# Performance work log

Measured on AMD Instinct MI355X. Metric: run time of the kernel, lower is better.

## Reference

```python
import jax, jax.numpy as jnp
import numpy as np


def setup_inputs() -> dict:
    key = jax.random.key(0)
    k0, k1, k2, k3 = jax.random.split(key, 4)
    B, in_dim, n_vars, out_dim, E = 64, 512, 512, 720, 8
    x = jax.random.normal(k0, (B, in_dim, n_vars), dtype=jnp.float32)
    # Gating: nn.Linear(in_dim, E, bias=False) -> weight [E, in_dim]
    Wg = jax.random.normal(k1, (E, in_dim), dtype=jnp.float32) * 0.02
    # Experts: nn.Linear(in_dim, out_dim) -> weight [out_dim, in_dim], bias [out_dim]
    We = jax.random.normal(k2, (E, out_dim, in_dim), dtype=jnp.float32) * 0.02
    be = jax.random.normal(k3, (E, out_dim), dtype=jnp.float32) * 0.02
    return {"x": x, "Wg": Wg, "We": We, "be": be, "top_k": 2}


def reference(x, Wg, We, be, top_k):
    # x: [B, in_len, n_vars] -> tokens along n_vars with feature dim in_len
    xt = jnp.swapaxes(x, 1, 2)                      # [B, V, D]
    gate = jax.nn.softmax(xt @ Wg.T, axis=-1)       # [B, V, E]
    weights, sel = jax.lax.top_k(gate, top_k)       # [B, V, k]
    E, O, D = We.shape
    out = jnp.zeros(xt.shape[:2] + (O,), dtype=xt.dtype)  # [B, V, O]
    for e in range(E):
        # combine weight for expert e: sum over top-k slots routed to e
        coef = jnp.sum(jnp.where(sel == e, weights, jnp.zeros_like(weights)), axis=-1)  # [B, V]
        out = out + coef[..., None] * (jnp.einsum('bvd,od->bvo', xt, We[e]) + be[e])
    return jnp.swapaxes(out, 1, 2)                  # [B, pred_len, n_vars]
```

## Files before the change

### kernel.cpp

```cpp
#include <hip/hip_runtime.h>
#include <hip/hip_bf16.h>

#define DID 512
#define NV  512
#define NB  64
#define OD  720
#define OPAD 768
#define NE  8
#define NTOK (NB * NV)
#define MAXTILE 512

typedef short  bf16x8 __attribute__((ext_vector_type(8)));
typedef float  f32x4  __attribute__((ext_vector_type(4)));

#define XT_OFF    0u
#define WB_OFF    33554432u
#define PID_OFF   39845888u
#define C1D_OFF   39976960u
#define C2D_OFF   40108032u
#define TL_OFF    40239104u
#define CL1_OFF   40370176u
#define CL2_OFF   40501248u
#define BCNT_OFF  40632320u
#define BFILL_OFF 40632576u
#define BOFF_OFF  40632832u
#define TPID_OFF  40633088u
#define TT0_OFF   40635136u
#define TEND_OFF  40637184u
#define NT_OFF    40639232u
#define SCR_OFF   40639488u
#define SCR_END   87825408u

static __device__ __forceinline__ ushort f2bf(float f) {
  unsigned u = __float_as_uint(f);
  unsigned r = (u + 0x7fffu + ((u >> 16) & 1u)) >> 16;
  return (ushort)r;
}
static __device__ __forceinline__ float bf2f(ushort u) {
  return __uint_as_float(((unsigned)u) << 16);
}
static __device__ __forceinline__ void async16(const ushort* g, ushort* l) {
  __builtin_amdgcn_global_load_lds((__attribute__((address_space(1))) void*)(g),
                                   (__attribute__((address_space(3))) void*)(l),
                                   16, 0, 0);
}

__global__ __launch_bounds__(256) void k_prep(const float* __restrict__ x,
                                              ushort* __restrict__ xt,
                                              const float* __restrict__ We,
                                              ushort* __restrict__ wb,
                                              int* __restrict__ bcnt) {
  const int tid = threadIdx.x;
  if (blockIdx.z < 64) {
    if (blockIdx.z == 0 && blockIdx.x == 0 && blockIdx.y == 0 && tid < 128)
      bcnt[tid] = 0;
    __shared__ float s[32][33];
    const int b  = blockIdx.z;
    const int v0 = blockIdx.x * 32;
    const int d0 = blockIdx.y * 32;
    const int tx = tid & 31;
    const int ty = tid >> 5;
    const float* xp = x + ((size_t)b * DID + d0 + ty) * NV + v0 + tx;
#pragma unroll
    for (int i = 0; i < 4; ++i) s[ty + i * 8][tx] = xp[(size_t)i * 8 * NV];
    __syncthreads();
#pragma unroll
    for (int i = 0; i < 4; ++i) {
      int vl = ty + i * 8;
      xt[((size_t)b * NV + v0 + vl) * DID + d0 + tx] = f2bf(s[tx][vl]);
    }
  } else {
    const int e = blockIdx.z - 64;
    int i = (blockIdx.y * 16 + blockIdx.x) * 256 + tid;
    for (; i < OPAD * DID; i += 65536) {
      const int o = i >> 9;
      ushort val = 0;
      if (o < OD) val = f2bf(We[(size_t)e * OD * DID + i]);
      wb[(size_t)e * OPAD * DID + i] = val;
    }
  }
}

__global__ __launch_bounds__(256) void k_gate(const float* __restrict__ x,
                                              const float* __restrict__ Wg,
                                              int* __restrict__ pairid,
                                              float* __restrict__ c1d,
                                              float* __restrict__ c2d,
                                              int* __restrict__ bcnt) {
  __shared__ float wg[NE * DID];
  __shared__ int cnt64[64];
  const int tid = threadIdx.x;
  for (int i = tid; i < NE * DID; i += 256) wg[i] = Wg[i];
  if (tid < 64) cnt64[tid] = 0;
  __syncthreads();

  const int b = blockIdx.y;
  const int v = blockIdx.x * 256 + tid;
  const float* xp = x + (size_t)b * DID * NV + v;

  float acc[NE];
#pragma unroll
  for (int e = 0; e < NE; ++e) acc[e] = 0.f;
  for (int d = 0; d < DID; d += 4) {
    float x0 = xp[(size_t)(d + 0) * NV];
    float x1 = xp[(size_t)(d + 1) * NV];
    float x2 = xp[(size_t)(d + 2) * NV];
    float x3 = xp[(size_t)(d + 3) * NV];
#pragma unroll
    for (int e = 0; e < NE; ++e) {
      float4 w4 = *(const float4*)&wg[e * DID + d];
      acc[e] += x0 * w4.x + x1 * w4.y + x2 * w4.z + x3 * w4.w;
    }
  }
  float mx = acc[0];
#pragma unroll
  for (int e = 1; e < NE; ++e) mx = fmaxf(mx, acc[e]);
  float sum = 0.f;
#pragma unroll
  for (int e = 0; e < NE; ++e) { acc[e] = __expf(acc[e] - mx); sum += acc[e]; }
  const float inv = 1.f / sum;

  int i1 = 0; float g1 = acc[0];
#pragma unroll
  for (int e = 1; e < NE; ++e) if (acc[e] > g1) { g1 = acc[e]; i1 = e; }
  int i2 = -1; float g2 = -1.f;
#pragma unroll
  for (int e = 0; e < NE; ++e) if (e != i1 && acc[e] > g2) { g2 = acc[e]; i2 = e; }
  g1 *= inv; g2 *= inv;

  int ea, eb; float ca, cb;
  if (i1 < i2) { ea = i1; eb = i2; ca = g1; cb = g2; }
  else         { ea = i2; eb = i1; ca = g2; cb = g1; }
  const int pid = ea * 8 + eb;
  const int t = b * NV + v;
  pairid[t] = pid; c1d[t] = ca; c2d[t] = cb;
  atomicAdd(&cnt64[pid], 1);
  __syncthreads();
  if (tid < 64 && cnt64[tid]) atomicAdd(&bcnt[tid], cnt64[tid]);
}

__global__ void k_prefix(const int* __restrict__ bcnt, int* __restrict__ boffs,
                         int* __restrict__ tpid, int* __restrict__ tt0,
                         int* __restrict__ tend, int* __restrict__ ntp) {
  const int p = threadIdx.x;
  const int c = bcnt[p];
  int inc = c;
#pragma unroll
  for (int d = 1; d < 64; d <<= 1) {
    int n = __shfl_up(inc, d, 64);
    if (p >= d) inc += n;
  }
  const int off = inc - c;
  boffs[p] = off;
  const int tc = (c + 127) >> 7;
  int inct = tc;
#pragma unroll
  for (int d = 1; d < 64; d <<= 1) {
    int n = __shfl_up(inct, d, 64);
    if (p >= d) inct += n;
  }
  const int tb = inct - tc;
  for (int i = 0; i < tc; ++i) {
    tpid[tb + i] = p; tt0[tb + i] = off + i * 128; tend[tb + i] = off + c;
  }
  if (p == 63) ntp[0] = inct;
}

__global__ __launch_bounds__(256) void k_scatter(const int* __restrict__ pairid,
                                                 const float* __restrict__ c1d,
                                                 const float* __restrict__ c2d,
                                                 const int* __restrict__ boffs,
                                                 int* __restrict__ bfill,
                                                 int* __restrict__ tlist,
                                                 float* __restrict__ cl1,
                                                 float* __restrict__ cl2) {
  __shared__ int cnt64[64], base64[64];
  const int tid = threadIdx.x;
  if (tid < 64) cnt64[tid] = 0;
  __syncthreads();
  const int t = blockIdx.x * 256 + tid;
  const int pid = pairid[t];
  const int p = atomicAdd(&cnt64[pid], 1);
  __syncthreads();
  if (tid < 64) base64[tid] = cnt64[tid] ? atomicAdd(&bfill[tid], cnt64[tid]) : 0;
  __syncthreads();
  const int slot = boffs[pid] + base64[pid] + p;
  tlist[slot] = t; cl1[slot] = c1d[t]; cl2[slot] = c2d[t];
}

__global__ __launch_bounds__(256, 2) void k_gemm(
    const ushort* __restrict__ xt, const ushort* __restrict__ wb,
    const float* __restrict__ be, const int* __restrict__ tlist,
    const float* __restrict__ cl1, const float* __restrict__ cl2,
    const int* __restrict__ tpid, const int* __restrict__ tt0,
    const int* __restrict__ tendarr, const int* __restrict__ ntp,
    ushort* __restrict__ scratch, float* __restrict__ out, int mode) {
  const int tile = blockIdx.y;
  if (tile >= ntp[0]) return;
  const int pid  = tpid[tile];
  const int t0   = tt0[tile];
  const int tend = tendarr[tile];
  const int e1 = pid >> 3, e2 = pid & 7;
  const int o0 = blockIdx.x * 128;

  __shared__ __align__(16) ushort As[2][4096];
  __shared__ __align__(16) ushort Bs[2][4096];

  const int tid  = threadIdx.x;
  const int lane = tid & 63;
  const int w    = tid >> 6;
  const int m16  = lane & 15;
  const int ch   = lane >> 4;

  const int rA0 = 2 * w * 16 + m16;
  const int sl0 = t0 + rA0, sl1 = sl0 + 16;
  const int tk0 = (sl0 < tend) ? tlist[sl0] : 0;
  const int tk1 = (sl1 < tend) ? tlist[sl1] : 0;

  const size_t eStride = (size_t)OPAD * DID;
  const int    aoff    = (o0 + rA0) * DID + ch * 8;
  const ushort* gb0 = xt + (size_t)tk0 * DID + ch * 8;
  const ushort* gb1 = xt + (size_t)tk1 * DID + ch * 8;

  const int dst0 = 2 * w * 512 + lane * 8;
  const int dst1 = dst0 + 512;

  const int m    = lane & 15;
  const int quad = lane >> 4;
  const int wo   = (w >> 1) * 64;
  const int wt   = (w & 1) * 64;
  const int fa   = (w >> 1) * 4;
  const int fb   = (w & 1) * 4;

  f32x4 acc[4][4];
#pragma unroll
  for (int i = 0; i < 4; ++i)
#pragma unroll
    for (int j = 0; j < 4; ++j) acc[i][j] = (f32x4){0.f, 0.f, 0.f, 0.f};

  {
    const ushort* wA = wb + (size_t)e1 * eStride + aoff;
    async16(wA, &As[0][dst0]);
    async16(wA + 16 * DID, &As[0][dst1]);
    async16(gb0, &Bs[0][dst0]);
    async16(gb1, &Bs[0][dst1]);
  }

  for (int kk = 0; kk < 32; ++kk) {
    __syncthreads();

    if (kk == 16) {
      float ratio[4];
#pragma unroll
      for (int j = 0; j < 4; ++j) {
        const int sl = t0 + wt + j * 16 + m;
        const bool g = sl < tend;
        const float cc1 = g ? cl1[sl] : 0.f;
        const float cc2 = g ? cl2[sl] : 1.f;
        ratio[j] = cc1 / cc2;
      }
      const float* be1p = be + e1 * OD;
#pragma unroll
      for (int i = 0; i < 4; ++i) {
        const int ob = o0 + wo + i * 16 + quad * 4;
        float b0 = 0, b1 = 0, b2 = 0, b3 = 0;
        if (ob < OD) { b0 = be1p[ob]; b1 = be1p[ob + 1]; b2 = be1p[ob + 2]; b3 = be1p[ob + 3]; }
#pragma unroll
        for (int j = 0; j < 4; ++j) {
          acc[i][j][0] = (acc[i][j][0] + b0) * ratio[j];
          acc[i][j][1] = (acc[i][j][1] + b1) * ratio[j];
          acc[i][j][2] = (acc[i][j][2] + b2) * ratio[j];
          acc[i][j][3] = (acc[i][j][3] + b3) * ratio[j];
        }
      }
    }

    const int nk = kk + 1;
    if (nk < 32) {
      const int nb = nk & 1;
      const int eA = (nk < 16) ? e1 : e2;
      const int k0 = (nk & 15) * 32;
      const ushort* wA = wb + (size_t)eA * eStride + aoff + k0;
      async16(wA, &As[nb][dst0]);
      async16(wA + 16 * DID, &As[nb][dst1]);
      async16(gb0 + k0, &Bs[nb][dst0]);
      async16(gb1 + k0, &Bs[nb][dst1]);
    }

    const int cb = kk & 1;
    bf16x8 af[4], bfr[4];
#pragma unroll
    for (int i = 0; i < 4; ++i)
      af[i] = *(const bf16x8*)(&As[cb][(fa + i) * 512 + lane * 8]);
#pragma unroll
    for (int j = 0; j < 4; ++j)
      bfr[j] = *(const bf16x8*)(&Bs[cb][(fb + j) * 512 + lane * 8]);
#pragma unroll
    for (int i = 0; i < 4; ++i)
#pragma unroll
      for (int j = 0; j < 4; ++j)
        acc[i][j] = __builtin_amdgcn_mfma_f32_16x16x32_bf16(af[i], bfr[j],
                                                            acc[i][j], 0, 0, 0);
  }

  float c2v[4]; int tokv[4]; bool gv[4];
#pragma unroll
  for (int j = 0; j < 4; ++j) {
    const int sl = t0 + wt + j * 16 + m;
    gv[j] = sl < tend;
    c2v[j]  = gv[j] ? cl2[sl] : 0.f;
    tokv[j] = gv[j] ? tlist[sl] : 0;
  }
  const float* be2p = be + e2 * OD;
#pragma unroll
  for (int i = 0; i < 4; ++i) {
    const int ob = o0 + wo + i * 16 + quad * 4;
    if (ob < OD) {
      const float b0 = be2p[ob], b1 = be2p[ob + 1], b2 = be2p[ob + 2], b3 = be2p[ob + 3];
#pragma unroll
      for (int j = 0; j < 4; ++j) {
        if (gv[j]) {
          const float v0 = c2v[j] * (acc[i][j][0] + b0);
          const float v1 = c2v[j] * (acc[i][j][1] + b1);
          const float v2 = c2v[j] * (acc[i][j][2] + b2);
          const float v3 = c2v[j] * (acc[i][j][3] + b3);
          if (mode == 0) {
            ushort4 pk = make_ushort4(f2bf(v0), f2bf(v1), f2bf(v2), f2bf(v3));
            *(ushort4*)(scratch + (size_t)tokv[j] * OD + ob) = pk;
          } else {
            const int bb = tokv[j] >> 9, vv = tokv[j] & 511;
            float* op = out + ((size_t)bb * OD + ob) * NV + vv;
            op[0] = v0; op[(size_t)NV] = v1; op[2 * (size_t)NV] = v2; op[3 * (size_t)NV] = v3;
          }
        }
      }
    }
  }
}

__global__ __launch_bounds__(256) void k_combine(const ushort* __restrict__ scratch,
                                                 float* __restrict__ out) {
  __shared__ ushort s[64][68];
  const int v0 = blockIdx.x * 64;
  const int o0 = blockIdx.y * 64;
  const int b  = blockIdx.z;
  const int tid = threadIdx.x;
#pragma unroll
  for (int it = 0; it < 2; ++it) {
    const int c = it * 256 + tid;
    const int row = c >> 3, cg = c & 7;
    const int o = o0 + cg * 8;
    if (o + 8 <= OD) {
      const ushort* src = scratch + ((size_t)(b * NV + v0 + row)) * OD + o;
      ushort4 ua = *(const ushort4*)(src);
      ushort4 ub = *(const ushort4*)(src + 4);
      *(ushort4*)&s[row][cg * 8] = ua;
      *(ushort4*)&s[row][cg * 8 + 4] = ub;
    }
  }
  __syncthreads();
  const int vv = tid & 63;
  const int og = tid >> 6;
#pragma unroll
  for (int oi = 0; oi < 8; ++oi) {
    const int ol = (og * 8 + oi) * 2;
    const int o = o0 + ol;
    if (o < OD) {
      ushort2 u = *(const ushort2*)&s[vv][ol];
      float* op = out + ((size_t)b * OD + o) * NV + v0 + vv;
      op[0]  = bf2f(u.x);
      op[NV] = bf2f(u.y);
    }
  }
}

extern "C" void kernel_launch(void* const* d_in, const int* in_sizes, int n_in,
                              void* d_out, int out_size, void* d_ws, size_t ws_size,
                              hipStream_t stream) {
  const float* x  = (const float*)d_in[0];
  const float* Wg = (const float*)d_in[1];
  const float* We = (const float*)d_in[2];
  const float* be = (const float*)d_in[3];
  float* out = (float*)d_out;

  char* ws = (char*)d_ws;
  ushort* xt     = (ushort*)(ws + XT_OFF);
  ushort* wb     = (ushort*)(ws + WB_OFF);
  int*    pairid = (int*)   (ws + PID_OFF);
  float*  c1d    = (float*) (ws + C1D_OFF);
  float*  c2d    = (float*) (ws + C2D_OFF);
  int*    tlist  = (int*)   (ws + TL_OFF);
  float*  cl1    = (float*) (ws + CL1_OFF);
  float*  cl2    = (float*) (ws + CL2_OFF);
  int*    bcnt   = (int*)   (ws + BCNT_OFF);
  int*    bfill  = (int*)   (ws + BFILL_OFF);
  int*    boffs  = (int*)   (ws + BOFF_OFF);
  int*    tpid   = (int*)   (ws + TPID_OFF);
  int*    tt0    = (int*)   (ws + TT0_OFF);
  int*    tend   = (int*)   (ws + TEND_OFF);
  int*    ntp    = (int*)   (ws + NT_OFF);
  ushort* scratch= (ushort*)(ws + SCR_OFF);

  const int mode = (ws_size >= (size_t)SCR_END) ? 0 : 1;

  k_prep<<<dim3(16, 16, 72), 256, 0, stream>>>(x, xt, We, wb, bcnt);
  k_gate<<<dim3(NV / 256, NB), 256, 0, stream>>>(x, Wg, pairid, c1d, c2d, bcnt);
  k_prefix<<<1, 64, 0, stream>>>(bcnt, boffs, tpid, tt0, tend, ntp);
  k_scatter<<<NTOK / 256, 256, 0, stream>>>(pairid, c1d, c2d, boffs, bfill,
                                            tlist, cl1, cl2);
  k_gemm<<<dim3(OPAD / 128, 320), 256, 0, stream>>>(xt, wb, be, tlist, cl1, cl2,
                                                    tpid, tt0, tend, ntp,
                                                    scratch, out, mode);
  if (mode == 0)
    k_combine<<<dim3(NV / 64, (OD + 63) / 64, NB), 256, 0, stream>>>(scratch, out);
}
```

Before: 359.2 us.

## Write GEMM output directly, drop bf16 scratch combine pass, widen transpose tiles

Drops the bf16 scratch buffer and the separate combine/transpose kernel. The GEMM epilogue now always scatters fp32 results straight into the transposed output. The grid is swapped so that consecutive blocks walk token tiles instead of output columns. The x transpose-and-convert in k_prep moves to 64x64 tiles with 4-wide packed bf16 stores, and the We conversion uses fewer blocks. This trades the extra kernel launch and the scratch round trip for strided, uncoalesced fp32 stores from the GEMM.

```diff
diff --git a/kernel.cpp b/kernel.cpp
--- a/kernel.cpp
+++ b/kernel.cpp
@@ -28,16 +28,11 @@
 #define TT0_OFF   40635136u
 #define TEND_OFF  40637184u
 #define NT_OFF    40639232u
-#define SCR_OFF   40639488u
-#define SCR_END   87825408u
 
 static __device__ __forceinline__ ushort f2bf(float f) {
   unsigned u = __float_as_uint(f);
   unsigned r = (u + 0x7fffu + ((u >> 16) & 1u)) >> 16;
   return (ushort)r;
-}
-static __device__ __forceinline__ float bf2f(ushort u) {
-  return __uint_as_float(((unsigned)u) << 16);
 }
 static __device__ __forceinline__ void async16(const ushort* g, ushort* l) {
   __builtin_amdgcn_global_load_lds((__attribute__((address_space(1))) void*)(g),
@@ -54,25 +49,30 @@
   if (blockIdx.z < 64) {
     if (blockIdx.z == 0 && blockIdx.x == 0 && blockIdx.y == 0 && tid < 128)
       bcnt[tid] = 0;
-    __shared__ float s[32][33];
+    __shared__ float s[64][65];
     const int b  = blockIdx.z;
-    const int v0 = blockIdx.x * 32;
-    const int d0 = blockIdx.y * 32;
-    const int tx = tid & 31;
-    const int ty = tid >> 5;
-    const float* xp = x + ((size_t)b * DID + d0 + ty) * NV + v0 + tx;
-#pragma unroll
-    for (int i = 0; i < 4; ++i) s[ty + i * 8][tx] = xp[(size_t)i * 8 * NV];
+    const int v0 = blockIdx.x * 64;
+    const int d0 = blockIdx.y * 64;
+    const int vx = tid & 63;
+    const int dy = tid >> 6;
+    const float* xp = x + ((size_t)b * DID + d0 + dy) * NV + v0 + vx;
+#pragma unroll
+    for (int i = 0; i < 16; ++i)
+      s[dy + i * 4][vx] = xp[(size_t)i * 4 * NV];
     __syncthreads();
-#pragma unroll
-    for (int i = 0; i < 4; ++i) {
-      int vl = ty + i * 8;
-      xt[((size_t)b * NV + v0 + vl) * DID + d0 + tx] = f2bf(s[tx][vl]);
+    const int dg = tid & 15;
+    const int vr = tid >> 4;
+#pragma unroll
+    for (int p = 0; p < 4; ++p) {
+      const int v = p * 16 + vr;
+      ushort4 pk = make_ushort4(f2bf(s[dg * 4 + 0][v]), f2bf(s[dg * 4 + 1][v]),
+                                f2bf(s[dg * 4 + 2][v]), f2bf(s[dg * 4 + 3][v]));
+      *(ushort4*)&xt[((size_t)b * NV + v0 + v) * DID + d0 + dg * 4] = pk;
     }
   } else {
     const int e = blockIdx.z - 64;
-    int i = (blockIdx.y * 16 + blockIdx.x) * 256 + tid;
-    for (; i < OPAD * DID; i += 65536) {
+    int i = (blockIdx.y * 8 + blockIdx.x) * 256 + tid;
+    for (; i < OPAD * DID; i += 16384) {
       const int o = i >> 9;
       ushort val = 0;
       if (o < OD) val = f2bf(We[(size_t)e * OD * DID + i]);
@@ -194,14 +194,14 @@
     const float* __restrict__ cl1, const float* __restrict__ cl2,
     const int* __restrict__ tpid, const int* __restrict__ tt0,
     const int* __restrict__ tendarr, const int* __restrict__ ntp,
-    ushort* __restrict__ scratch, float* __restrict__ out, int mode) {
-  const int tile = blockIdx.y;
+    float* __restrict__ out) {
+  const int tile = blockIdx.x;
   if (tile >= ntp[0]) return;
   const int pid  = tpid[tile];
   const int t0   = tt0[tile];
   const int tend = tendarr[tile];
   const int e1 = pid >> 3, e2 = pid & 7;
-  const int o0 = blockIdx.x * 128;
+  const int o0 = blockIdx.y * 128;
 
   __shared__ __align__(16) ushort As[2][4096];
   __shared__ __align__(16) ushort Bs[2][4096];
@@ -320,56 +320,14 @@
 #pragma unroll
       for (int j = 0; j < 4; ++j) {
         if (gv[j]) {
-          const float v0 = c2v[j] * (acc[i][j][0] + b0);
-          const float v1 = c2v[j] * (acc[i][j][1] + b1);
-          const float v2 = c2v[j] * (acc[i][j][2] + b2);
-          const float v3 = c2v[j] * (acc[i][j][3] + b3);
-          if (mode == 0) {
-            ushort4 pk = make_ushort4(f2bf(v0), f2bf(v1), f2bf(v2), f2bf(v3));
-            *(ushort4*)(scratch + (size_t)tokv[j] * OD + ob) = pk;
-          } else {
-            const int bb = tokv[j] >> 9, vv = tokv[j] & 511;
-            float* op = out + ((size_t)bb * OD + ob) * NV + vv;
-            op[0] = v0; op[(size_t)NV] = v1; op[2 * (size_t)NV] = v2; op[3 * (size_t)NV] = v3;
-          }
+          const int bb = tokv[j] >> 9, vv = tokv[j] & 511;
+          float* op = out + ((size_t)bb * OD + ob) * NV + vv;
+          op[0]              = c2v[j] * (acc[i][j][0] + b0);
+          op[(size_t)NV]     = c2v[j] * (acc[i][j][1] + b1);
+          op[2 * (size_t)NV] = c2v[j] * (acc[i][j][2] + b2);
+          op[3 * (size_t)NV] = c2v[j] * (acc[i][j][3] + b3);
         }
       }
-    }
-  }
-}
-
-__global__ __launch_bounds__(256) void k_combine(const ushort* __restrict__ scratch,
-                                                 float* __restrict__ out) {
-  __shared__ ushort s[64][68];
-  const int v0 = blockIdx.x * 64;
-  const int o0 = blockIdx.y * 64;
-  const int b  = blockIdx.z;
-  const int tid = threadIdx.x;
-#pragma unroll
-  for (int it = 0; it < 2; ++it) {
-    const int c = it * 256 + tid;
-    const int row = c >> 3, cg = c & 7;
-    const int o = o0 + cg * 8;
-    if (o + 8 <= OD) {
-      const ushort* src = scratch + ((size_t)(b * NV + v0 + row)) * OD + o;
-      ushort4 ua = *(const ushort4*)(src);
-      ushort4 ub = *(const ushort4*)(src + 4);
-      *(ushort4*)&s[row][cg * 8] = ua;
-      *(ushort4*)&s[row][cg * 8 + 4] = ub;
-    }
-  }
-  __syncthreads();
-  const int vv = tid & 63;
-  const int og = tid >> 6;
-#pragma unroll
-  for (int oi = 0; oi < 8; ++oi) {
-    const int ol = (og * 8 + oi) * 2;
-    const int o = o0 + ol;
-    if (o < OD) {
-      ushort2 u = *(const ushort2*)&s[vv][ol];
-      float* op = out + ((size_t)b * OD + o) * NV + v0 + vv;
-      op[0]  = bf2f(u.x);
-      op[NV] = bf2f(u.y);
     }
   }
 }
@@ -399,18 +357,12 @@
   int*    tt0    = (int*)   (ws + TT0_OFF);
   int*    tend   = (int*)   (ws + TEND_OFF);
   int*    ntp    = (int*)   (ws + NT_OFF);
-  ushort* scratch= (ushort*)(ws + SCR_OFF);
-
-  const int mode = (ws_size >= (size_t)SCR_END) ? 0 : 1;
-
-  k_prep<<<dim3(16, 16, 72), 256, 0, stream>>>(x, xt, We, wb, bcnt);
+
+  k_prep<<<dim3(8, 8, 72), 256, 0, stream>>>(x, xt, We, wb, bcnt);
   k_gate<<<dim3(NV / 256, NB), 256, 0, stream>>>(x, Wg, pairid, c1d, c2d, bcnt);
   k_prefix<<<1, 64, 0, stream>>>(bcnt, boffs, tpid, tt0, tend, ntp);
   k_scatter<<<NTOK / 256, 256, 0, stream>>>(pairid, c1d, c2d, boffs, bfill,
                                             tlist, cl1, cl2);
-  k_gemm<<<dim3(OPAD / 128, 320), 256, 0, stream>>>(xt, wb, be, tlist, cl1, cl2,
-                                                    tpid, tt0, tend, ntp,
-                                                    scratch, out, mode);
-  if (mode == 0)
-    k_combine<<<dim3(NV / 64, (OD + 63) / 64, NB), 256, 0, stream>>>(scratch, out);
-}
+  k_gemm<<<dim3(320, OPAD / 128), 256, 0, stream>>>(xt, wb, be, tlist, cl1, cl2,
+                                                    tpid, tt0, tend, ntp, out);
+}
```

After: 519.4 us. +44.6%, slower.
